# Kernel tuning notes

Hardware: AMD Instinct MI355X
Metric: run time of the kernel (lower is better)

The kernel has to match this reference:

```python
import jax, jax.numpy as jnp
import numpy as np

B, H, S, D = 2, 12, 4096, 64

def setup_inputs() -> dict:
    key = jax.random.key(0)
    kq, kk, kv = jax.random.split(key, 3)
    Q = jax.random.normal(kq, (B, H, S, D), dtype=jnp.float32)
    K = jax.random.normal(kk, (B, H, S, D), dtype=jnp.float32)
    V = jax.random.normal(kv, (B, H, S, D), dtype=jnp.float32)
    attn_mask = jnp.zeros((1, 1, 1, 1), dtype=bool)  # unused by the original forward
    return {"Q": Q, "K": K, "V": V, "attn_mask": attn_mask}

def reference(Q, K, V, attn_mask):
    d_k = K.shape[3]
    # scores: [B, H, S, S] -- naive full materialization, matching the original
    scores = jnp.einsum("bhqd,bhkd->bhqk", Q, K) / np.sqrt(d_k).astype(Q.dtype)
    attn = jax.nn.softmax(scores, axis=-1)
    context = jnp.einsum("bhqk,bhkd->bhqd", attn, V)
    return context
```

## Files before the change

kernel.cpp:

```cpp
#include <hip/hip_runtime.h>

typedef _Float16 half4_t __attribute__((ext_vector_type(4)));
typedef _Float16 half8_t __attribute__((ext_vector_type(8)));
typedef float floatx4 __attribute__((ext_vector_type(4)));

constexpr int S_  = 4096;
constexpr int D_  = 64;
constexpr int NBH = 24;
constexpr float SC2 = 0.125f * 1.44269504088896340736f;

__device__ __forceinline__ void async16(const _Float16* g, _Float16* l) {
  __builtin_amdgcn_global_load_lds((const __attribute__((address_space(1))) void*)g,
                                   (__attribute__((address_space(3))) void*)l, 16, 0, 0);
}

__global__ __launch_bounds__(256) void preconv(
    const float* __restrict__ K, const float* __restrict__ V,
    _Float16* __restrict__ Kh, _Float16* __restrict__ Vh)
{
  __shared__ float tile[64 * 68];
  const int lin = blockIdx.x;
  const int xcd = lin & 7;
  const int idx = lin >> 3;
  const int bh  = xcd * 3 + (idx >> 6);
  const int kt  = idx & 63;
  const int tid = threadIdx.x;
  const size_t tbase = ((size_t)bh * 64 + kt) * 4096;
#pragma unroll
  for (int it = 0; it < 2; ++it) {
    size_t i = tbase + (size_t)(tid + 256 * it) * 8;
    float4 a = *(const float4*)(K + i);
    float4 b = *(const float4*)(K + i + 4);
    *(half8_t*)(Kh + i) = (half8_t){
      (_Float16)(a.x*SC2),(_Float16)(a.y*SC2),(_Float16)(a.z*SC2),(_Float16)(a.w*SC2),
      (_Float16)(b.x*SC2),(_Float16)(b.y*SC2),(_Float16)(b.z*SC2),(_Float16)(b.w*SC2) };
  }
#pragma unroll
  for (int it = 0; it < 4; ++it) {
    int r  = (tid >> 4) + 16 * it;
    int c4 = (tid & 15) * 4;
    *(float4*)(&tile[r * 68 + c4]) = *(const float4*)(V + tbase + (size_t)r * 64 + c4);
  }
  __syncthreads();
  const int d = tid >> 2;
  _Float16 out[16];
#pragma unroll
  for (int j = 0; j < 16; ++j)
    out[j] = (_Float16)tile[((tid & 3) * 16 + j) * 68 + d];
  _Float16* dst = Vh + tbase + (size_t)d * 64 + (tid & 3) * 16;
  *(half8_t*)(dst)     = *(half8_t*)(&out[0]);
  *(half8_t*)(dst + 8) = *(half8_t*)(&out[8]);
}


__global__ __launch_bounds__(256, 3) void fattn3(
    const float* __restrict__ Qf, const _Float16* __restrict__ Kh,
    const _Float16* __restrict__ Vh, float* __restrict__ O)
{
  __shared__ __align__(16) _Float16 smem[3 * 8192 + 512];

  const int tid  = threadIdx.x;
  const int lane = tid & 63;
  const int w    = tid >> 6;
  const int g    = lane >> 4;
  const int m    = lane & 15;

  const int bid  = blockIdx.x;
  const int xcd  = bid & 7;
  const int slot = bid >> 3;
  const int bh   = xcd * 3 + (slot >> 6);
  const int qblk = slot & 63;
  const size_t base = (size_t)bh * S_ * D_;
  const int q0 = qblk * 64;

  half8_t qf[4][2];
#pragma unroll
  for (int qt = 0; qt < 4; ++qt)
#pragma unroll
    for (int ks = 0; ks < 2; ++ks) {
      const float4* qp = (const float4*)(Qf + base + (size_t)(q0 + qt*16 + m) * D_ + 8*g + 32*ks);
      float4 a = qp[0], b = qp[1];
      qf[qt][ks] = (half8_t){ (_Float16)a.x,(_Float16)a.y,(_Float16)a.z,(_Float16)a.w,
                              (_Float16)b.x,(_Float16)b.y,(_Float16)b.z,(_Float16)b.w };
    }

  floatx4 oacc[4][4];
#pragma unroll
  for (int qt = 0; qt < 4; ++qt)
#pragma unroll
    for (int db = 0; db < 4; ++db) oacc[qt][db] = (floatx4){0.f,0.f,0.f,0.f};
  float lsum[4] = {0.f, 0.f, 0.f, 0.f};

  const int krow_s  = lane >> 3;
  const int kchunk  = (lane & 7) ^ (krow_s & 7);
  const int kg1 = (16*w + krow_s) * 64 + kchunk * 8;
  const int kg2 = kg1 + 8 * 64;
  const int vd   = lane >> 1;
  const int vgc  = (lane & 1) ^ (vd & 1);
  const int vg1 = vd * 64 + (2*w + vgc) * 8;
  const int vg2 = vg1 + 32 * 64;

  const _Float16* Kb = Kh + base;
  const _Float16* Vb = Vh + base;
  const int wbase = w * 2048;

  auto stage = [&](int bufoff, int kt) {
    const _Float16* Kt = Kb + ((size_t)kt << 12);
    const _Float16* Vt = Vb + ((size_t)kt << 12);
    _Float16* s = smem + bufoff + wbase;
    async16(Kt + kg1, s);
    async16(Kt + kg2, s + 512);
    async16(Vt + vg1, s + 1024);
    async16(Vt + vg2, s + 1536);
  };

  int b0 = 0, b1 = 8192, b2 = 16384;
  stage(b0, 0);
  stage(b1, 1);

  for (int kt = 0; kt < 64; ++kt) {
    stage(b2, (kt + 2) & 63);
    asm volatile("s_waitcnt vmcnt(8)" ::: "memory");

    const _Float16* Kd = smem + b0 + wbase;
    const _Float16* Vd = Kd + 1024;

    half8_t kf0 = *(const half8_t*)(&Kd[m * 64 + ((g    ) ^ (m & 7)) * 8]);
    half8_t kf1 = *(const half8_t*)(&Kd[m * 64 + ((g + 4) ^ (m & 7)) * 8]);
    half4_t vf[4];
#pragma unroll
    for (int db = 0; db < 4; ++db)
      vf[db] = *(const half4_t*)(&Vd[(16*db + m) * 16 + (((g >> 1) ^ (m & 1)) * 8) + (g & 1) * 4]);

#pragma unroll
    for (int qt = 0; qt < 4; ++qt) {
      floatx4 s0 = (floatx4){0.f,0.f,0.f,0.f};
      s0 = __builtin_amdgcn_mfma_f32_16x16x32_f16(kf0, qf[qt][0], s0, 0, 0, 0);
      s0 = __builtin_amdgcn_mfma_f32_16x16x32_f16(kf1, qf[qt][1], s0, 0, 0, 0);

      float p0 = __builtin_amdgcn_exp2f(s0[0]);
      float p1 = __builtin_amdgcn_exp2f(s0[1]);
      float p2 = __builtin_amdgcn_exp2f(s0[2]);
      float p3 = __builtin_amdgcn_exp2f(s0[3]);
      lsum[qt] += (p0 + p1) + (p2 + p3);
      half4_t pf = (half4_t){ (_Float16)p0, (_Float16)p1, (_Float16)p2, (_Float16)p3 };

#pragma unroll
      for (int db = 0; db < 4; ++db)
        oacc[qt][db] = __builtin_amdgcn_mfma_f32_16x16x16f16(pf, vf[db], oacc[qt][db], 0, 0, 0);
    }

    int t = b0; b0 = b1; b1 = b2; b2 = t;
  }

  asm volatile("s_waitcnt vmcnt(0)" ::: "memory");
  __syncthreads();
  float* red  = (float*)smem;
  float* lred = red + 12288;

#pragma unroll
  for (int qt = 0; qt < 4; ++qt) {
    float l = lsum[qt];
    l += __shfl_xor(l, 16);
    l += __shfl_xor(l, 32);
    lsum[qt] = l;
  }

  if (w > 0) {
#pragma unroll
    for (int qt = 0; qt < 4; ++qt) {
#pragma unroll
      for (int db = 0; db < 4; ++db)
        *(floatx4*)(&red[(w-1)*4096 + (qt*4 + db)*256 + lane*4]) = oacc[qt][db];
      lred[(w-1)*64 + qt*16 + m] = lsum[qt];
    }
  }
  __syncthreads();
  if (w == 0) {
#pragma unroll
    for (int qt = 0; qt < 4; ++qt) {
#pragma unroll
      for (int db = 0; db < 4; ++db) {
#pragma unroll
        for (int p = 0; p < 3; ++p)
          oacc[qt][db] += *(const floatx4*)(&red[p*4096 + (qt*4 + db)*256 + lane*4]);
      }
      float l = lsum[qt] + lred[qt*16 + m] + lred[64 + qt*16 + m] + lred[128 + qt*16 + m];
      floatx4 linv;
#pragma unroll
      for (int r = 0; r < 4; ++r)
        linv[r] = 1.0f / __shfl(l, (lane & 48) + 4*g + r);
      float* Op = O + base + (size_t)(q0 + qt*16) * D_;
#pragma unroll
      for (int db = 0; db < 4; ++db)
#pragma unroll
        for (int r = 0; r < 4; ++r)
          Op[(size_t)(4*g + r) * D_ + 16*db + m] = oacc[qt][db][r] * linv[r];
    }
  }
}

constexpr int SKf = 72;
constexpr int SVf = 68;
__global__ __launch_bounds__(256, 3) void fattn_fb(
    const float* __restrict__ Q, const float* __restrict__ K,
    const float* __restrict__ V, float* __restrict__ O)
{
  __shared__ __align__(16) _Float16 Ks[2][64 * SKf];
  __shared__ __align__(16) _Float16 Vs[2][64 * SVf];
  const int tid = threadIdx.x, lane = tid & 63, w = tid >> 6, g = lane >> 4, m = lane & 15;
  const int bid = blockIdx.x, xcd = bid & 7, slot = bid >> 3;
  const int bh = xcd * 3 + (slot >> 5), qblk = slot & 31;
  const size_t base = (size_t)bh * S_ * D_;
  const int q0 = qblk * 128 + w * 32;
  half8_t qf[2][2];
#pragma unroll
  for (int qt = 0; qt < 2; ++qt)
#pragma unroll
    for (int ks = 0; ks < 2; ++ks) {
      const float4* qp = (const float4*)(Q + base + (size_t)(q0 + qt*16 + m) * D_ + 8*g + 32*ks);
      float4 a = qp[0], b = qp[1];
      qf[qt][ks] = (half8_t){ (_Float16)(a.x*SC2),(_Float16)(a.y*SC2),(_Float16)(a.z*SC2),(_Float16)(a.w*SC2),
                              (_Float16)(b.x*SC2),(_Float16)(b.y*SC2),(_Float16)(b.z*SC2),(_Float16)(b.w*SC2) };
    }
  floatx4 oacc[2][4];
#pragma unroll
  for (int qt = 0; qt < 2; ++qt)
#pragma unroll
    for (int db = 0; db < 4; ++db) oacc[qt][db] = (floatx4){0.f,0.f,0.f,0.f};
  float lsum[2] = {0.f, 0.f};
  const float* Kb = K + base; const float* Vb = V + base;
  float4 kreg[4]; float vreg[16];
  const int sL = ((lane >> 2) ^ (lane >> 4)) & 3;
  auto issue = [&](int kt) {
    const float* Kt = Kb + (size_t)kt * 64 * D_;
#pragma unroll
    for (int it = 0; it < 2; ++it) {
      int sl = tid + 256*it; int key = sl >> 3; int c8 = (sl & 7) << 3;
      const float4* p = (const float4*)(Kt + (size_t)key * D_ + c8);
      kreg[2*it] = p[0]; kreg[2*it+1] = p[1];
    }
    const float* Vt = Vb + (size_t)kt * 64 * D_;
#pragma unroll
    for (int it = 0; it < 4; ++it) {
      int kb = it * 16 + (w << 2);
      const float* vp = Vt + (size_t)kb * D_ + lane;
      vreg[4*it+0]=vp[0]; vreg[4*it+1]=vp[D_]; vreg[4*it+2]=vp[2*D_]; vreg[4*it+3]=vp[3*D_];
    }
  };
  auto commit = [&](int buf) {
    _Float16* Kd = Ks[buf]; _Float16* Vd = Vs[buf];
#pragma unroll
    for (int it = 0; it < 2; ++it) {
      int sl = tid + 256*it; int key = sl >> 3; int c8 = (sl & 7) << 3;
      float4 a = kreg[2*it], b = kreg[2*it+1];
      *(half8_t*)(&Kd[key * SKf + c8]) = (half8_t){ (_Float16)a.x,(_Float16)a.y,(_Float16)a.z,(_Float16)a.w,
                                                    (_Float16)b.x,(_Float16)b.y,(_Float16)b.z,(_Float16)b.w };
    }
#pragma unroll
    for (int it = 0; it < 4; ++it)
      *(half4_t*)(&Vd[lane * SVf + 4 * ((4*it + w) ^ sL)]) =
        (half4_t){ (_Float16)vreg[4*it+0], (_Float16)vreg[4*it+1], (_Float16)vreg[4*it+2], (_Float16)vreg[4*it+3] };
  };
  issue(0); commit(0); __syncthreads();
  const int s0i = m >> 2;
  for (int kt = 0; kt < 64; ++kt) {
    const int cur = kt & 1;
    if (kt < 63) issue(kt + 1);
    const _Float16* Kd = Ks[cur]; const _Float16* Vd = Vs[cur];
    half8_t kf[4][2];
#pragma unroll
    for (int nb = 0; nb < 4; ++nb) {
      kf[nb][0] = *(const half8_t*)(&Kd[(16*nb + m) * SKf + 8*g]);
      kf[nb][1] = *(const half8_t*)(&Kd[(16*nb + m) * SKf + 8*g + 32]);
    }
    half4_t vf[4][4];
#pragma unroll
    for (int nb = 0; nb < 4; ++nb)
#pragma unroll
      for (int db = 0; db < 4; ++db)
        vf[nb][db] = *(const half4_t*)(&Vd[(16*db + m) * SVf + 4 * ((4*nb + g) ^ s0i ^ db)]);
#pragma unroll
    for (int qt = 0; qt < 2; ++qt) {
      floatx4 sacc[4];
#pragma unroll
      for (int nb = 0; nb < 4; ++nb) {
        floatx4 acc = (floatx4){0.f,0.f,0.f,0.f};
        acc = __builtin_amdgcn_mfma_f32_16x16x32_f16(kf[nb][0], qf[qt][0], acc, 0, 0, 0);
        acc = __builtin_amdgcn_mfma_f32_16x16x32_f16(kf[nb][1], qf[qt][1], acc, 0, 0, 0);
        sacc[nb] = acc;
      }
      half4_t pf[4]; float ls = 0.f;
#pragma unroll
      for (int nb = 0; nb < 4; ++nb) {
        float p0 = __builtin_amdgcn_exp2f(sacc[nb][0]); float p1 = __builtin_amdgcn_exp2f(sacc[nb][1]);
        float p2 = __builtin_amdgcn_exp2f(sacc[nb][2]); float p3 = __builtin_amdgcn_exp2f(sacc[nb][3]);
        ls += p0 + p1 + p2 + p3;
        pf[nb] = (half4_t){ (_Float16)p0, (_Float16)p1, (_Float16)p2, (_Float16)p3 };
      }
      lsum[qt] += ls;
#pragma unroll
      for (int nb = 0; nb < 4; ++nb)
#pragma unroll
        for (int db = 0; db < 4; ++db)
          oacc[qt][db] = __builtin_amdgcn_mfma_f32_16x16x16f16(pf[nb], vf[nb][db], oacc[qt][db], 0, 0, 0);
    }
    if (kt < 63) commit(1 - cur);
    __syncthreads();
  }
#pragma unroll
  for (int qt = 0; qt < 2; ++qt) {
    float l = lsum[qt];
    l += __shfl_xor(l, 16); l += __shfl_xor(l, 32);
    floatx4 linv;
#pragma unroll
    for (int r = 0; r < 4; ++r) linv[r] = 1.0f / __shfl(l, (lane & 48) + 4*g + r);
    float* Op = O + base + (size_t)(q0 + qt*16) * D_;
#pragma unroll
    for (int db = 0; db < 4; ++db)
#pragma unroll
      for (int r = 0; r < 4; ++r)
        Op[(size_t)(4*g + r) * D_ + 16*db + m] = oacc[qt][db][r] * linv[r];
  }
}

extern "C" void kernel_launch(void* const* d_in, const int* in_sizes, int n_in,
                              void* d_out, int out_size, void* d_ws, size_t ws_size,
                              hipStream_t stream) {
  const float* Q = (const float*)d_in[0];
  const float* K = (const float*)d_in[1];
  const float* V = (const float*)d_in[2];
  float* Out = (float*)d_out;

  constexpr size_t NELEM = (size_t)NBH * S_ * D_;
  constexpr size_t NEED  = 2 * NELEM * sizeof(_Float16);

  if (ws_size >= NEED) {
    _Float16* Khp = (_Float16*)d_ws;
    _Float16* Vhp = Khp + NELEM;
    preconv<<<NBH * 64, 256, 0, stream>>>(K, V, Khp, Vhp);
    fattn3<<<NBH * 64, 256, 0, stream>>>(Q, Khp, Vhp, Out);
  } else {
    fattn_fb<<<NBH * 32, 256, 0, stream>>>(Q, K, V, Out);
  }
}
```

Before: 247.9 us.

## Load K/V fragments directly into registers with MFMA-ready V layout

The preconversion kernel now writes V in a fragment-ordered layout so each lane can load its MFMA operands with plain 16-byte global loads. The attention kernel drops the async global-to-LDS triple-buffered pipeline and instead double-buffers K/V fragments in registers, prefetching the next tile while computing the current one. The cross-wave reduction becomes a two-step tree using a smaller shared buffer. This removes LDS traffic and LDS reads from the hot loop, at the cost of more registers and relying on L2/cache for latency hiding.

Result: slower. 291.8 us (+17.7%).

```diff
diff --git a/kernel.cpp b/kernel.cpp
--- a/kernel.cpp
+++ b/kernel.cpp
@@ -8,11 +8,6 @@
 constexpr int D_  = 64;
 constexpr int NBH = 24;
 constexpr float SC2 = 0.125f * 1.44269504088896340736f;
-
-__device__ __forceinline__ void async16(const _Float16* g, _Float16* l) {
-  __builtin_amdgcn_global_load_lds((const __attribute__((address_space(1))) void*)g,
-                                   (__attribute__((address_space(3))) void*)l, 16, 0, 0);
-}
 
 __global__ __launch_bounds__(256) void preconv(
     const float* __restrict__ K, const float* __restrict__ V,
@@ -42,22 +37,26 @@
     *(float4*)(&tile[r * 68 + c4]) = *(const float4*)(V + tbase + (size_t)r * 64 + c4);
   }
   __syncthreads();
-  const int d = tid >> 2;
-  _Float16 out[16];
-#pragma unroll
-  for (int j = 0; j < 16; ++j)
-    out[j] = (_Float16)tile[((tid & 3) * 16 + j) * 68 + d];
-  _Float16* dst = Vh + tbase + (size_t)d * 64 + (tid & 3) * 16;
-  *(half8_t*)(dst)     = *(half8_t*)(&out[0]);
-  *(half8_t*)(dst + 8) = *(half8_t*)(&out[8]);
+#pragma unroll
+  for (int j = 0; j < 2; ++j) {
+    int c   = tid * 2 + j;
+    int d15 = c >> 5, dbp = (c >> 4) & 1, kg = c & 15;
+    _Float16 out[8];
+#pragma unroll
+    for (int dblo = 0; dblo < 2; ++dblo)
+#pragma unroll
+      for (int r = 0; r < 4; ++r)
+        out[dblo*4 + r] = (_Float16)tile[(4*kg + r) * 68 + 32*dbp + 16*dblo + d15];
+    *(half8_t*)(Vh + tbase + (size_t)c * 8) = *(half8_t*)out;
+  }
 }
 
 
-__global__ __launch_bounds__(256, 3) void fattn3(
+__global__ __launch_bounds__(256, 3) void fattn4(
     const float* __restrict__ Qf, const _Float16* __restrict__ Kh,
     const _Float16* __restrict__ Vh, float* __restrict__ O)
 {
-  __shared__ __align__(16) _Float16 smem[3 * 8192 + 512];
+  __shared__ float red[8192 + 256];
 
   const int tid  = threadIdx.x;
   const int lane = tid & 63;
@@ -91,111 +90,114 @@
     for (int db = 0; db < 4; ++db) oacc[qt][db] = (floatx4){0.f,0.f,0.f,0.f};
   float lsum[4] = {0.f, 0.f, 0.f, 0.f};
 
-  const int krow_s  = lane >> 3;
-  const int kchunk  = (lane & 7) ^ (krow_s & 7);
-  const int kg1 = (16*w + krow_s) * 64 + kchunk * 8;
-  const int kg2 = kg1 + 8 * 64;
-  const int vd   = lane >> 1;
-  const int vgc  = (lane & 1) ^ (vd & 1);
-  const int vg1 = vd * 64 + (2*w + vgc) * 8;
-  const int vg2 = vg1 + 32 * 64;
-
   const _Float16* Kb = Kh + base;
   const _Float16* Vb = Vh + base;
-  const int wbase = w * 2048;
-
-  auto stage = [&](int bufoff, int kt) {
-    const _Float16* Kt = Kb + ((size_t)kt << 12);
-    const _Float16* Vt = Vb + ((size_t)kt << 12);
-    _Float16* s = smem + bufoff + wbase;
-    async16(Kt + kg1, s);
-    async16(Kt + kg2, s + 512);
-    async16(Vt + vg1, s + 1024);
-    async16(Vt + vg2, s + 1536);
-  };
-
-  int b0 = 0, b1 = 8192, b2 = 16384;
-  stage(b0, 0);
-  stage(b1, 1);
-
-  for (int kt = 0; kt < 64; ++kt) {
-    stage(b2, (kt + 2) & 63);
-    asm volatile("s_waitcnt vmcnt(8)" ::: "memory");
-
-    const _Float16* Kd = smem + b0 + wbase;
-    const _Float16* Vd = Kd + 1024;
-
-    half8_t kf0 = *(const half8_t*)(&Kd[m * 64 + ((g    ) ^ (m & 7)) * 8]);
-    half8_t kf1 = *(const half8_t*)(&Kd[m * 64 + ((g + 4) ^ (m & 7)) * 8]);
-    half4_t vf[4];
-#pragma unroll
-    for (int db = 0; db < 4; ++db)
-      vf[db] = *(const half4_t*)(&Vd[(16*db + m) * 16 + (((g >> 1) ^ (m & 1)) * 8) + (g & 1) * 4]);
-
+  const int ko0 = (16*w + m) * 64 + 8*g;
+  const int ko1 = ko0 + 32;
+  const int vo0 = (m*2 + 0) * 128 + (4*w + g) * 8;
+  const int vo1 = (m*2 + 1) * 128 + (4*w + g) * 8;
+
+  half8_t ka0, ka1, va0, va1, kb0, kb1, vb0, vb1;
+
+  ka0 = *(const half8_t*)(Kb + ko0);
+  ka1 = *(const half8_t*)(Kb + ko1);
+  va0 = *(const half8_t*)(Vb + vo0);
+  va1 = *(const half8_t*)(Vb + vo1);
+
+  auto compute = [&](half8_t k0, half8_t k1, half8_t v0, half8_t v1) {
+    half4_t vf0 = (half4_t){v0[0], v0[1], v0[2], v0[3]};
+    half4_t vf1 = (half4_t){v0[4], v0[5], v0[6], v0[7]};
+    half4_t vf2 = (half4_t){v1[0], v1[1], v1[2], v1[3]};
+    half4_t vf3 = (half4_t){v1[4], v1[5], v1[6], v1[7]};
 #pragma unroll
     for (int qt = 0; qt < 4; ++qt) {
-      floatx4 s0 = (floatx4){0.f,0.f,0.f,0.f};
-      s0 = __builtin_amdgcn_mfma_f32_16x16x32_f16(kf0, qf[qt][0], s0, 0, 0, 0);
-      s0 = __builtin_amdgcn_mfma_f32_16x16x32_f16(kf1, qf[qt][1], s0, 0, 0, 0);
-
-      float p0 = __builtin_amdgcn_exp2f(s0[0]);
-      float p1 = __builtin_amdgcn_exp2f(s0[1]);
-      float p2 = __builtin_amdgcn_exp2f(s0[2]);
-      float p3 = __builtin_amdgcn_exp2f(s0[3]);
+      floatx4 s = (floatx4){0.f,0.f,0.f,0.f};
+      s = __builtin_amdgcn_mfma_f32_16x16x32_f16(k0, qf[qt][0], s, 0, 0, 0);
+      s = __builtin_amdgcn_mfma_f32_16x16x32_f16(k1, qf[qt][1], s, 0, 0, 0);
+      float p0 = __builtin_amdgcn_exp2f(s[0]);
+      float p1 = __builtin_amdgcn_exp2f(s[1]);
+      float p2 = __builtin_amdgcn_exp2f(s[2]);
+      float p3 = __builtin_amdgcn_exp2f(s[3]);
       lsum[qt] += (p0 + p1) + (p2 + p3);
       half4_t pf = (half4_t){ (_Float16)p0, (_Float16)p1, (_Float16)p2, (_Float16)p3 };
-
-#pragma unroll
-      for (int db = 0; db < 4; ++db)
-        oacc[qt][db] = __builtin_amdgcn_mfma_f32_16x16x16f16(pf, vf[db], oacc[qt][db], 0, 0, 0);
-    }
-
-    int t = b0; b0 = b1; b1 = b2; b2 = t;
-  }
-
-  asm volatile("s_waitcnt vmcnt(0)" ::: "memory");
-  __syncthreads();
-  float* red  = (float*)smem;
-  float* lred = red + 12288;
-
+      oacc[qt][0] = __builtin_amdgcn_mfma_f32_16x16x16f16(pf, vf0, oacc[qt][0], 0, 0, 0);
+      oacc[qt][1] = __builtin_amdgcn_mfma_f32_16x16x16f16(pf, vf1, oacc[qt][1], 0, 0, 0);
+      oacc[qt][2] = __builtin_amdgcn_mfma_f32_16x16x16f16(pf, vf2, oacc[qt][2], 0, 0, 0);
+      oacc[qt][3] = __builtin_amdgcn_mfma_f32_16x16x16f16(pf, vf3, oacc[qt][3], 0, 0, 0);
+    }
+  };
+
+  for (int kt = 0; kt < 64; kt += 2) {
+    {
+      const _Float16* Kt = Kb + ((size_t)((kt + 1) & 63) << 12);
+      const _Float16* Vt = Vb + ((size_t)((kt + 1) & 63) << 12);
+      kb0 = *(const half8_t*)(Kt + ko0);
+      kb1 = *(const half8_t*)(Kt + ko1);
+      vb0 = *(const half8_t*)(Vt + vo0);
+      vb1 = *(const half8_t*)(Vt + vo1);
+    }
+    compute(ka0, ka1, va0, va1);
+    {
+      const _Float16* Kt = Kb + ((size_t)((kt + 2) & 63) << 12);
+      const _Float16* Vt = Vb + ((size_t)((kt + 2) & 63) << 12);
+      ka0 = *(const half8_t*)(Kt + ko0);
+      ka1 = *(const half8_t*)(Kt + ko1);
+      va0 = *(const half8_t*)(Vt + vo0);
+      va1 = *(const half8_t*)(Vt + vo1);
+    }
+    compute(kb0, kb1, vb0, vb1);
+  }
+
+  float* lred = red + 8192;
 #pragma unroll
   for (int qt = 0; qt < 4; ++qt) {
     float l = lsum[qt];
     l += __shfl_xor(l, 16);
     l += __shfl_xor(l, 32);
     lsum[qt] = l;
-  }
-
-  if (w > 0) {
-#pragma unroll
-    for (int qt = 0; qt < 4; ++qt) {
+    lred[w*64 + qt*16 + m] = l;
+  }
+  if (w >= 2) {
+#pragma unroll
+    for (int qt = 0; qt < 4; ++qt)
 #pragma unroll
       for (int db = 0; db < 4; ++db)
-        *(floatx4*)(&red[(w-1)*4096 + (qt*4 + db)*256 + lane*4]) = oacc[qt][db];
-      lred[(w-1)*64 + qt*16 + m] = lsum[qt];
-    }
+        *(floatx4*)(&red[(w-2)*4096 + (qt*4 + db)*256 + lane*4]) = oacc[qt][db];
+  }
+  __syncthreads();
+  if (w < 2) {
+#pragma unroll
+    for (int qt = 0; qt < 4; ++qt)
+#pragma unroll
+      for (int db = 0; db < 4; ++db)
+        oacc[qt][db] += *(const floatx4*)(&red[w*4096 + (qt*4 + db)*256 + lane*4]);
+  }
+  __syncthreads();
+  if (w == 1) {
+#pragma unroll
+    for (int qt = 0; qt < 4; ++qt)
+#pragma unroll
+      for (int db = 0; db < 4; ++db)
+        *(floatx4*)(&red[(qt*4 + db)*256 + lane*4]) = oacc[qt][db];
   }
   __syncthreads();
   if (w == 0) {
 #pragma unroll
     for (int qt = 0; qt < 4; ++qt) {
-#pragma unroll
-      for (int db = 0; db < 4; ++db) {
-#pragma unroll
-        for (int p = 0; p < 3; ++p)
-          oacc[qt][db] += *(const floatx4*)(&red[p*4096 + (qt*4 + db)*256 + lane*4]);
-      }
-      float l = lsum[qt] + lred[qt*16 + m] + lred[64 + qt*16 + m] + lred[128 + qt*16 + m];
+      float l = lred[qt*16 + m] + lred[64 + qt*16 + m]
+              + lred[128 + qt*16 + m] + lred[192 + qt*16 + m];
       floatx4 linv;
 #pragma unroll
       for (int r = 0; r < 4; ++r)
         linv[r] = 1.0f / __shfl(l, (lane & 48) + 4*g + r);
       float* Op = O + base + (size_t)(q0 + qt*16) * D_;
 #pragma unroll
-      for (int db = 0; db < 4; ++db)
+      for (int db = 0; db < 4; ++db) {
+        floatx4 o = oacc[qt][db] + *(const floatx4*)(&red[(qt*4 + db)*256 + lane*4]);
 #pragma unroll
         for (int r = 0; r < 4; ++r)
-          Op[(size_t)(4*g + r) * D_ + 16*db + m] = oacc[qt][db][r] * linv[r];
+          Op[(size_t)(4*g + r) * D_ + 16*db + m] = o[r] * linv[r];
+      }
     }
   }
 }
@@ -339,7 +341,7 @@
     _Float16* Khp = (_Float16*)d_ws;
     _Float16* Vhp = Khp + NELEM;
     preconv<<<NBH * 64, 256, 0, stream>>>(K, V, Khp, Vhp);
-    fattn3<<<NBH * 64, 256, 0, stream>>>(Q, Khp, Vhp, Out);
+    fattn4<<<NBH * 64, 256, 0, stream>>>(Q, Khp, Vhp, Out);
   } else {
     fattn_fb<<<NBH * 32, 256, 0, stream>>>(Q, K, V, Out);
   }
```
